# Optimization experiments

Measured on AMD Instinct MI355X. Metric: run time of the kernel, lower is better.

Reference implementation:

```python
import jax, jax.numpy as jnp
import numpy as np


def setup_inputs() -> dict:
    key = jax.random.key(0)
    ks = jax.random.split(key, 3)
    B, d_in, d_latent = 8192, 768, 12288
    x = jax.random.normal(ks[0], (B, d_in), dtype=jnp.float32)
    # kaiming_normal fan_in relu: std = sqrt(2/d_in)
    W_enc = jax.random.normal(ks[1], (d_latent, d_in), dtype=jnp.float32) * np.sqrt(2.0 / d_in)
    b_enc = jnp.zeros((d_latent,), dtype=jnp.float32)
    # xavier_normal: std = sqrt(2/(d_in+d_latent))
    W_dec = jax.random.normal(ks[2], (d_in, d_latent), dtype=jnp.float32) * np.sqrt(2.0 / (d_in + d_latent))
    b_dec = jnp.zeros((d_in,), dtype=jnp.float32)
    b_pre = jnp.zeros((d_in,), dtype=jnp.float32)
    return {"x": x, "b_pre": b_pre, "W_enc": W_enc, "b_enc": b_enc,
            "W_dec": W_dec, "b_dec": b_dec, "k": 64}


def reference(x, b_pre, W_enc, b_enc, W_dec, b_dec, k):
    # encode: a = (x - b_pre) @ W_enc.T + b_enc   -> (B, d_latent)
    x0 = x - b_pre
    a = jnp.einsum('bi,li->bl', x0, W_enc) + b_enc
    # topk activation (mode='value', nonneg=True): relu then keep k largest
    a_relu = jax.nn.relu(a)
    topk_val, topk_idx = jax.lax.top_k(a_relu, k)  # (B, k)
    B = a.shape[0]
    rows = jnp.arange(B)[:, None]
    z = jnp.zeros_like(a).at[rows, topk_idx].set(topk_val)
    # decode: x_hat = z @ W_dec.T + b_dec
    x_hat = jnp.einsum('bl,il->bi', z, W_dec) + b_dec
    return (x_hat, z, a)
```

## Files before the change

### kernel.cpp

```cpp
#include <hip/hip_runtime.h>

#define DIN 768
#define DL  12288
#define CAP 320
#define MARGIN 0.03f
#define UB 0.015f
#define UMAX 64
#define KMAX 128

typedef __attribute__((ext_vector_type(8))) _Float16 half8;
typedef __attribute__((ext_vector_type(4))) _Float16 half4v;
typedef __attribute__((ext_vector_type(4))) float f32x4;

__device__ __forceinline__ void gl_lds16(const void* g, void* s) {
  __builtin_amdgcn_global_load_lds(
      (const __attribute__((address_space(1))) unsigned int*)g,
      (__attribute__((address_space(3))) unsigned int*)s, 16, 0, 0);
}
__device__ __forceinline__ void wait_lgkm0_fence() {
  asm volatile("s_waitcnt lgkmcnt(0)" ::: "memory");
  __builtin_amdgcn_sched_barrier(0);
}
__device__ __forceinline__ void wait_vm0() {
  asm volatile("s_waitcnt vmcnt(0)" ::: "memory");
}

__global__ __launch_bounds__(256) void k_split_x(const float* __restrict__ x,
    const float* __restrict__ b_pre, _Float16* __restrict__ Ah)
{
  const int i4 = blockIdx.x * 256 + threadIdx.x;
  const int col4 = (i4 % (DIN / 4)) * 4;
  const float4 xv = *(const float4*)&x[(size_t)i4 * 4];
  const float4 bp = *(const float4*)&b_pre[col4];
  half4v o;
  o.x = (_Float16)(xv.x - bp.x);
  o.y = (_Float16)(xv.y - bp.y);
  o.z = (_Float16)(xv.z - bp.z);
  o.w = (_Float16)(xv.w - bp.w);
  *(half4v*)&Ah[(size_t)i4 * 4] = o;
}

__global__ __launch_bounds__(256) void k_split_w(const float* __restrict__ W,
                                                 _Float16* __restrict__ Bh)
{
  const int i4 = blockIdx.x * 256 + threadIdx.x;
  const float4 wv = *(const float4*)&W[(size_t)i4 * 4];
  half4v o;
  o.x = (_Float16)wv.x; o.y = (_Float16)wv.y;
  o.z = (_Float16)wv.z; o.w = (_Float16)wv.w;
  *(half4v*)&Bh[(size_t)i4 * 4] = o;
}

__global__ __launch_bounds__(256) void k_transpose(const float* __restrict__ W,
                                                   _Float16* __restrict__ WT)
{
  __shared__ float t[32][33];
  const int c0 = blockIdx.x * 32;
  const int r0 = blockIdx.y * 32;
  const int x = threadIdx.x;
  const int y = threadIdx.y;
#pragma unroll
  for (int dy = 0; dy < 32; dy += 8)
    t[y + dy][x] = W[(size_t)(r0 + y + dy) * DL + c0 + x];
  __syncthreads();
#pragma unroll
  for (int dy = 0; dy < 32; dy += 8)
    WT[(size_t)(c0 + y + dy) * DIN + r0 + x] = (_Float16)t[x][y + dy];
}

#define BM 256
#define BN 256
#define BKE 64
#define NKT (DIN / BKE)

__global__ __launch_bounds__(512) void k_encode_f16(
    const _Float16* __restrict__ Ah, const _Float16* __restrict__ Bh,
    const float* __restrict__ b_enc, float* __restrict__ aout)
{
  __shared__ _Float16 sA[2][BM][BKE];
  __shared__ _Float16 sB[2][BN][BKE];
  const int tid = threadIdx.x, wave = tid >> 6, lane = tid & 63;
  const int wm = wave >> 2, wn = wave & 3;
  const int fr = lane & 15, fc = lane >> 4;

  const int q = ((8192 / BM) * (DL / BN)) >> 3;
  const int wg = (blockIdx.x & 7) * q + (blockIdx.x >> 3);
  const int bm = (wg / (DL / BN)) * BM;
  const int bn = (wg % (DL / BN)) * BN;

  const int lrow = lane >> 3;
  const int lcol = ((lane & 7) ^ lrow) << 3;
  const _Float16* gA = Ah + (size_t)(bm + lrow) * DIN + lcol;
  const _Float16* gB = Bh + (size_t)(bn + lrow) * DIN + lcol;

  f32x4 acc[8][4];
#pragma unroll
  for (int i = 0; i < 8; ++i)
#pragma unroll
    for (int j = 0; j < 4; ++j) acc[i][j] = f32x4{0.f, 0.f, 0.f, 0.f};

#define STAGE_TILE(buf, tt)                                                      \
  {                                                                              \
    _Pragma("unroll")                                                            \
    for (int s4 = 0; s4 < 4; ++s4) {                                             \
      const int s8 = (wave + s4 * 8) * 8;                                        \
      gl_lds16(gA + (size_t)s8 * DIN + (tt) * BKE, &sA[buf][s8][0]);             \
      gl_lds16(gB + (size_t)s8 * DIN + (tt) * BKE, &sB[buf][s8][0]);             \
    }                                                                            \
  }

#define LOADQ(p, mh, nh)                                                         \
  {                                                                              \
    const char* bA = (const char*)&sA[p][0][0];                                  \
    const char* bB = (const char*)&sB[p][0][0];                                  \
    _Pragma("unroll")                                                            \
    for (int i = 0; i < 4; ++i)                                                  \
      _Pragma("unroll")                                                          \
      for (int ks = 0; ks < 2; ++ks) {                                           \
        const int row = wm * 128 + ((mh) * 4 + i) * 16 + fr;                     \
        const int ph = (ks * 4 + fc) ^ (fr & 7);                                 \
        af[i][ks] = *(const half8*)(bA + row * (BKE * 2) + ph * 16);             \
      }                                                                          \
    _Pragma("unroll")                                                            \
    for (int j = 0; j < 2; ++j)                                                  \
      _Pragma("unroll")                                                          \
      for (int ks = 0; ks < 2; ++ks) {                                           \
        const int row = wn * 64 + ((nh) * 2 + j) * 16 + fr;                      \
        const int ph = (ks * 4 + fc) ^ (fr & 7);                                 \
        bf[j][ks] = *(const half8*)(bB + row * (BKE * 2) + ph * 16);             \
      }                                                                          \
  }

#define MFMAQ(mh, nh)                                                            \
  __builtin_amdgcn_s_setprio(1);                                                 \
  _Pragma("unroll")                                                              \
  for (int i = 0; i < 4; ++i)                                                    \
    _Pragma("unroll")                                                            \
    for (int j = 0; j < 2; ++j)                                                  \
      _Pragma("unroll")                                                          \
      for (int ks = 0; ks < 2; ++ks)                                             \
        acc[(mh) * 4 + i][(nh) * 2 + j] = __builtin_amdgcn_mfma_f32_16x16x32_f16( \
            af[i][ks], bf[j][ks], acc[(mh) * 4 + i][(nh) * 2 + j], 0, 0, 0);     \
  __builtin_amdgcn_s_setprio(0);

  half8 af[4][2], bf[2][2];

  STAGE_TILE(0, 0)
  wait_vm0();
  __builtin_amdgcn_s_barrier();

#pragma unroll 1
  for (int t = 0; t < NKT; ++t) {
    const int p = t & 1;
    LOADQ(p, 0, 0)
    if (t + 1 < NKT) STAGE_TILE(p ^ 1, t + 1)
    __builtin_amdgcn_s_barrier();
    wait_lgkm0_fence();
    MFMAQ(0, 0)
    __builtin_amdgcn_s_barrier();
    LOADQ(p, 0, 1)
    __builtin_amdgcn_s_barrier();
    wait_lgkm0_fence();
    MFMAQ(0, 1)
    __builtin_amdgcn_s_barrier();
    LOADQ(p, 1, 0)
    __builtin_amdgcn_s_barrier();
    wait_lgkm0_fence();
    MFMAQ(1, 0)
    __builtin_amdgcn_s_barrier();
    LOADQ(p, 1, 1)
    wait_vm0();
    __builtin_amdgcn_s_barrier();
    wait_lgkm0_fence();
    MFMAQ(1, 1)
    __builtin_amdgcn_s_barrier();
  }

#pragma unroll
  for (int j = 0; j < 4; ++j) {
    const int col = bn + wn * 64 + j * 16 + fr;
    const float be = b_enc[col];
#pragma unroll
    for (int i = 0; i < 8; ++i) {
      const int row0 = bm + wm * 128 + i * 16 + fc * 4;
#pragma unroll
      for (int r = 0; r < 4; ++r)
        aout[(size_t)(row0 + r) * DL + col] = acc[i][j][r] + be;
    }
  }
#undef STAGE_TILE
#undef LOADQ
#undef MFMAQ
}

__global__ __launch_bounds__(256) void k_fused(
    const float* __restrict__ a, const float* __restrict__ x,
    const float* __restrict__ b_pre, const float* __restrict__ W,
    const float* __restrict__ b_enc, const int* __restrict__ kp,
    const _Float16* __restrict__ WT, const float* __restrict__ b_dec,
    float* __restrict__ z, float* __restrict__ xhat)
{
  const int row = blockIdx.x, tid = threadIdx.x;
  const int wave = tid >> 6, lane = tid & 63;
  const int kk = min(max(kp[0], 1), KMAX);
  const float* ar = a + (size_t)row * DL;
  float* zr = z + (size_t)row * DL;

  __shared__ unsigned hist[4][512];
  __shared__ float s_wmax[4];
  __shared__ unsigned s_wsuf[4];
  __shared__ float s_Tm;
  __shared__ int s_cnt;
  __shared__ int cidx[CAP];
  __shared__ float caf[CAP];
  __shared__ double x0[DIN];
  __shared__ float s_ak;
  __shared__ int s_ucnt, s_nw;
  __shared__ int uidx[UMAX];
  __shared__ double uex[UMAX];
  __shared__ int widx[KMAX];
  __shared__ float wval[KMAX];

  float4 v[12];
#pragma unroll
  for (int j = 0; j < 12; ++j) {
    float4 t4 = ((const float4*)ar)[tid + 256 * j];
    t4.x = fmaxf(t4.x, 0.f); t4.y = fmaxf(t4.y, 0.f);
    t4.z = fmaxf(t4.z, 0.f); t4.w = fmaxf(t4.w, 0.f);
    v[j] = t4;
    const float4 zz = {0.f, 0.f, 0.f, 0.f};
    ((float4*)zr)[tid + 256 * j] = zz;
  }
  float m = 0.f;
#pragma unroll
  for (int j = 0; j < 12; ++j)
    m = fmaxf(m, fmaxf(fmaxf(v[j].x, v[j].y), fmaxf(v[j].z, v[j].w)));
#pragma unroll
  for (int off = 32; off; off >>= 1) m = fmaxf(m, __shfl_xor(m, off));
  if (lane == 0) s_wmax[wave] = m;
  if (tid == 0) { s_cnt = 0; s_Tm = -1.f; s_ak = -1e30f; s_ucnt = 0; s_nw = 0; }
  __syncthreads();
  const float rmax = fmaxf(fmaxf(s_wmax[0], s_wmax[1]), fmaxf(s_wmax[2], s_wmax[3]));

  float Tm;
  if (rmax <= 0.f) {
    Tm = 1e30f;
  } else {
    const float scale = 512.f / rmax;
    unsigned need = (unsigned)kk;
    bool found = false;
    for (int phase = 0; phase < 2 && !found; ++phase) {
      for (int i = tid; i < 4 * 512; i += 256) (&hist[0][0])[i] = 0u;
      __syncthreads();
      unsigned* h = hist[wave];
      const float sc = (phase == 0) ? scale : scale * 8.f;
#pragma unroll
      for (int j = 0; j < 12; ++j) {
        const float vv[4] = {v[j].x, v[j].y, v[j].z, v[j].w};
#pragma unroll
        for (int e = 0; e < 4; ++e) {
          const float val = vv[e];
          if (val > 0.f) {
            const float fb = val * scale;
            if (phase == 0) {
              if (fb >= 64.f) atomicAdd(&h[min(511, (int)fb)], 1u);
            } else {
              if (fb < 64.f) atomicAdd(&h[min(511, (int)(val * sc))], 1u);
            }
          }
        }
      }
      __syncthreads();
      const unsigned lo = hist[0][2 * tid] + hist[1][2 * tid] + hist[2][2 * tid] + hist[3][2 * tid];
      const unsigned hi = hist[0][2 * tid + 1] + hist[1][2 * tid + 1] + hist[2][2 * tid + 1] + hist[3][2 * tid + 1];
      const unsigned st = lo + hi;
      unsigned s = st;
#pragma unroll
      for (int off = 1; off < 64; off <<= 1) {
        const unsigned o = __shfl_down(s, off);
        if (lane + off < 64) s += o;
      }
      if (lane == 0) s_wsuf[wave] = s;
      __syncthreads();
      unsigned above_w = 0;
#pragma unroll
      for (int w2 = 0; w2 < 4; ++w2) if (w2 > wave) above_w += s_wsuf[w2];
      const unsigned inc = s + above_w;
      const unsigned excl = inc - st;
      const unsigned total = s_wsuf[0] + s_wsuf[1] + s_wsuf[2] + s_wsuf[3];
      if (total >= need) {
        if (inc >= need && excl < need) {
          const int bin = (excl + hi >= need) ? (2 * tid + 1) : (2 * tid);
          s_Tm = (float)bin / sc - MARGIN;
        }
        found = true;
      } else {
        need -= total;
      }
      __syncthreads();
    }
    Tm = s_Tm;
  }

#pragma unroll
  for (int j = 0; j < 12; ++j) {
    const float vv[4] = {v[j].x, v[j].y, v[j].z, v[j].w};
#pragma unroll
    for (int e = 0; e < 4; ++e) {
      if (vv[e] > 0.f && vv[e] >= Tm) {
        const int p = atomicAdd(&s_cnt, 1);
        if (p < CAP) { cidx[p] = (tid + 256 * j) * 4 + e; caf[p] = vv[e]; }
      }
    }
  }
  for (int i = tid; i < DIN; i += 256)
    x0[i] = (double)x[(size_t)row * DIN + i] - (double)b_pre[i];
  __syncthreads();
  const int C = min(s_cnt, CAP);

  if (C > kk) {
    if (tid < C) {
      const float mv = caf[tid];
      const int mi = cidx[tid];
      int r = 0;
      for (int j = 0; j < C; ++j) {
        const float fj = caf[j];
        if (fj > mv || (fj == mv && cidx[j] < mi)) ++r;
      }
      if (r == kk - 1) s_ak = mv;
    }
    __syncthreads();
  }
  const float ak = s_ak;

  if (tid < C) {
    const float mv = caf[tid];
    if (C <= kk || mv > ak + UB) {
      const int p = atomicAdd(&s_nw, 1);
      widx[p] = cidx[tid]; wval[p] = mv;
    } else if (mv >= ak - UB) {
      const int p = atomicAdd(&s_ucnt, 1);
      if (p < UMAX) uidx[p] = cidx[tid];
    }
  }
  __syncthreads();
  const int ci = s_nw;
  const int ucnt = min(s_ucnt, UMAX);

  for (int c = wave; c < ucnt; c += 4) {
    const int idx = uidx[c];
    const float* wrow = W + (size_t)idx * DIN;
    double s = 0.0;
#pragma unroll
    for (int it = 0; it < DIN / 64; ++it)
      s = fma(x0[lane + it * 64], (double)wrow[lane + it * 64], s);
#pragma unroll
    for (int mm = 32; mm; mm >>= 1) s += __shfl_xor(s, mm);
    if (lane == 0) {
      const double e = s + (double)b_enc[idx];
      uex[c] = e > 0.0 ? e : 0.0;
    }
  }
  __syncthreads();

  const int utake = min(kk - ci, ucnt);
  if (tid < ucnt) {
    const double mv = uex[tid];
    const int mi = uidx[tid];
    int r = 0;
    for (int j = 0; j < ucnt; ++j) {
      const double fj = uex[j];
      if (fj > mv || (fj == mv && uidx[j] < mi)) ++r;
    }
    if (r < utake) {
      const int p = atomicAdd(&s_nw, 1);
      widx[p] = mi; wval[p] = (float)mv;
    }
  }
  __syncthreads();
  const int nW = s_nw;

  if (tid < nW) zr[widx[tid]] = wval[tid];

  if (tid < 192) {
    float4 acc = ((const float4*)b_dec)[tid];
    for (int j = 0; j < nW; ++j) {
      const float vv = wval[j];
      const half4v w4 = *(const half4v*)(WT + (size_t)widx[j] * DIN + tid * 4);
      acc.x = fmaf(vv, (float)w4.x, acc.x);
      acc.y = fmaf(vv, (float)w4.y, acc.y);
      acc.z = fmaf(vv, (float)w4.z, acc.z);
      acc.w = fmaf(vv, (float)w4.w, acc.w);
    }
    ((float4*)(xhat + (size_t)row * DIN))[tid] = acc;
  }
}

extern "C" void kernel_launch(void* const* d_in, const int* in_sizes, int n_in,
                              void* d_out, int out_size, void* d_ws, size_t ws_size,
                              hipStream_t stream)
{
  const float* x     = (const float*)d_in[0];
  const float* b_pre = (const float*)d_in[1];
  const float* W_enc = (const float*)d_in[2];
  const float* b_enc = (const float*)d_in[3];
  const float* W_dec = (const float*)d_in[4];
  const float* b_dec = (const float*)d_in[5];
  const int*   kp    = (const int*)d_in[6];
  const int M = in_sizes[0] / DIN;

  float* xhat = (float*)d_out;
  float* z    = xhat + (size_t)M * DIN;
  float* a    = z + (size_t)M * DL;

  const bool bigws = ws_size >= ((size_t)192 << 20);
  _Float16 *WT16, *Ah, *Bh;
  if (bigws) {
    WT16 = (_Float16*)((char*)d_ws + ((size_t)1 << 20));
    Ah   = (_Float16*)((char*)d_ws + ((size_t)64 << 20));
    Bh   = (_Float16*)((char*)d_ws + ((size_t)96 << 20));
  } else {
    WT16 = (_Float16*)z;
    Ah   = (_Float16*)(z + (size_t)12 * 1024 * 1024);
    Bh   = (_Float16*)(z + (size_t)20 * 1024 * 1024);
  }

  k_split_x<<<M * DIN / 1024, 256, 0, stream>>>(x, b_pre, Ah);
  k_split_w<<<DL * DIN / 1024, 256, 0, stream>>>(W_enc, Bh);
  k_transpose<<<dim3(DL / 32, DIN / 32), dim3(32, 8), 0, stream>>>(W_dec, WT16);
  k_encode_f16<<<(M / BM) * (DL / BN), 512, 0, stream>>>(Ah, Bh, b_enc, a);
  k_fused<<<M, 256, 0, stream>>>(a, x, b_pre, W_enc, b_enc, kp, WT16, b_dec, z, xhat);
}
```

Measured before the change: 732.1 us.

## Merge prep kernels into one launch and widen fused top-k block to 512

The three preprocessing kernels (x cast, W_enc cast, W_dec transpose) become a single launch that dispatches on block index, which removes two kernel launches and their tail gaps. The per-row fused top-k/decode kernel moves from 256 to 512 threads, so each thread holds 6 float4s instead of 12. The histogram scan now uses one bin per thread, with 8 waves sharing 4 histogram copies. This is meant to cut register pressure and per-thread serial work, at the cost of more atomic contention on the shared histograms and more block-level sync overhead.

Result: faster. 665.4 us (-9.1%).

```diff
diff --git a/kernel.cpp b/kernel.cpp
--- a/kernel.cpp
+++ b/kernel.cpp
@@ -25,47 +25,48 @@
   asm volatile("s_waitcnt vmcnt(0)" ::: "memory");
 }
 
-__global__ __launch_bounds__(256) void k_split_x(const float* __restrict__ x,
-    const float* __restrict__ b_pre, _Float16* __restrict__ Ah)
+#define NBX (8192 * DIN / 1024)
+#define NBW (DL * DIN / 1024)
+#define NBT ((DL / 32) * (DIN / 32))
+
+__global__ __launch_bounds__(256) void k_prep(
+    const float* __restrict__ x, const float* __restrict__ b_pre,
+    const float* __restrict__ W_enc, const float* __restrict__ W_dec,
+    _Float16* __restrict__ Ah, _Float16* __restrict__ Bh, _Float16* __restrict__ WT)
 {
-  const int i4 = blockIdx.x * 256 + threadIdx.x;
-  const int col4 = (i4 % (DIN / 4)) * 4;
-  const float4 xv = *(const float4*)&x[(size_t)i4 * 4];
-  const float4 bp = *(const float4*)&b_pre[col4];
-  half4v o;
-  o.x = (_Float16)(xv.x - bp.x);
-  o.y = (_Float16)(xv.y - bp.y);
-  o.z = (_Float16)(xv.z - bp.z);
-  o.w = (_Float16)(xv.w - bp.w);
-  *(half4v*)&Ah[(size_t)i4 * 4] = o;
-}
-
-__global__ __launch_bounds__(256) void k_split_w(const float* __restrict__ W,
-                                                 _Float16* __restrict__ Bh)
-{
-  const int i4 = blockIdx.x * 256 + threadIdx.x;
-  const float4 wv = *(const float4*)&W[(size_t)i4 * 4];
-  half4v o;
-  o.x = (_Float16)wv.x; o.y = (_Float16)wv.y;
-  o.z = (_Float16)wv.z; o.w = (_Float16)wv.w;
-  *(half4v*)&Bh[(size_t)i4 * 4] = o;
-}
-
-__global__ __launch_bounds__(256) void k_transpose(const float* __restrict__ W,
-                                                   _Float16* __restrict__ WT)
-{
-  __shared__ float t[32][33];
-  const int c0 = blockIdx.x * 32;
-  const int r0 = blockIdx.y * 32;
-  const int x = threadIdx.x;
-  const int y = threadIdx.y;
-#pragma unroll
-  for (int dy = 0; dy < 32; dy += 8)
-    t[y + dy][x] = W[(size_t)(r0 + y + dy) * DL + c0 + x];
-  __syncthreads();
-#pragma unroll
-  for (int dy = 0; dy < 32; dy += 8)
-    WT[(size_t)(c0 + y + dy) * DIN + r0 + x] = (_Float16)t[x][y + dy];
+  const int b = blockIdx.x, tid = threadIdx.x;
+  if (b < NBX) {
+    const int i4 = b * 256 + tid;
+    const int col4 = (i4 % (DIN / 4)) * 4;
+    const float4 xv = *(const float4*)&x[(size_t)i4 * 4];
+    const float4 bp = *(const float4*)&b_pre[col4];
+    half4v o;
+    o.x = (_Float16)(xv.x - bp.x);
+    o.y = (_Float16)(xv.y - bp.y);
+    o.z = (_Float16)(xv.z - bp.z);
+    o.w = (_Float16)(xv.w - bp.w);
+    *(half4v*)&Ah[(size_t)i4 * 4] = o;
+  } else if (b < NBX + NBW) {
+    const int i4 = (b - NBX) * 256 + tid;
+    const float4 wv = *(const float4*)&W_enc[(size_t)i4 * 4];
+    half4v o;
+    o.x = (_Float16)wv.x; o.y = (_Float16)wv.y;
+    o.z = (_Float16)wv.z; o.w = (_Float16)wv.w;
+    *(half4v*)&Bh[(size_t)i4 * 4] = o;
+  } else {
+    const int idx = b - NBX - NBW;
+    const int c0 = (idx % (DL / 32)) * 32;
+    const int r0 = (idx / (DL / 32)) * 32;
+    const int xx = tid & 31, yy = tid >> 5;
+    __shared__ float t[32][33];
+#pragma unroll
+    for (int dy = 0; dy < 32; dy += 8)
+      t[yy + dy][xx] = W_dec[(size_t)(r0 + yy + dy) * DL + c0 + xx];
+    __syncthreads();
+#pragma unroll
+    for (int dy = 0; dy < 32; dy += 8)
+      WT[(size_t)(c0 + yy + dy) * DIN + r0 + xx] = (_Float16)t[xx][yy + dy];
+  }
 }
 
 #define BM 256
@@ -193,7 +194,7 @@
 #undef MFMAQ
 }
 
-__global__ __launch_bounds__(256) void k_fused(
+__global__ __launch_bounds__(512) void k_fused(
     const float* __restrict__ a, const float* __restrict__ x,
     const float* __restrict__ b_pre, const float* __restrict__ W,
     const float* __restrict__ b_enc, const int* __restrict__ kp,
@@ -207,8 +208,8 @@
   float* zr = z + (size_t)row * DL;
 
   __shared__ unsigned hist[4][512];
-  __shared__ float s_wmax[4];
-  __shared__ unsigned s_wsuf[4];
+  __shared__ float s_wmax[8];
+  __shared__ unsigned s_wsuf[8];
   __shared__ float s_Tm;
   __shared__ int s_cnt;
   __shared__ int cidx[CAP];
@@ -221,26 +222,28 @@
   __shared__ int widx[KMAX];
   __shared__ float wval[KMAX];
 
-  float4 v[12];
-#pragma unroll
-  for (int j = 0; j < 12; ++j) {
-    float4 t4 = ((const float4*)ar)[tid + 256 * j];
+  float4 v[6];
+#pragma unroll
+  for (int j = 0; j < 6; ++j) {
+    float4 t4 = ((const float4*)ar)[tid + 512 * j];
     t4.x = fmaxf(t4.x, 0.f); t4.y = fmaxf(t4.y, 0.f);
     t4.z = fmaxf(t4.z, 0.f); t4.w = fmaxf(t4.w, 0.f);
     v[j] = t4;
     const float4 zz = {0.f, 0.f, 0.f, 0.f};
-    ((float4*)zr)[tid + 256 * j] = zz;
+    ((float4*)zr)[tid + 512 * j] = zz;
   }
   float m = 0.f;
 #pragma unroll
-  for (int j = 0; j < 12; ++j)
+  for (int j = 0; j < 6; ++j)
     m = fmaxf(m, fmaxf(fmaxf(v[j].x, v[j].y), fmaxf(v[j].z, v[j].w)));
 #pragma unroll
   for (int off = 32; off; off >>= 1) m = fmaxf(m, __shfl_xor(m, off));
   if (lane == 0) s_wmax[wave] = m;
   if (tid == 0) { s_cnt = 0; s_Tm = -1.f; s_ak = -1e30f; s_ucnt = 0; s_nw = 0; }
   __syncthreads();
-  const float rmax = fmaxf(fmaxf(s_wmax[0], s_wmax[1]), fmaxf(s_wmax[2], s_wmax[3]));
+  float rmax = s_wmax[0];
+#pragma unroll
+  for (int w2 = 1; w2 < 8; ++w2) rmax = fmaxf(rmax, s_wmax[w2]);
 
   float Tm;
   if (rmax <= 0.f) {
@@ -250,12 +253,12 @@
     unsigned need = (unsigned)kk;
     bool found = false;
     for (int phase = 0; phase < 2 && !found; ++phase) {
-      for (int i = tid; i < 4 * 512; i += 256) (&hist[0][0])[i] = 0u;
+      for (int i = tid; i < 4 * 512; i += 512) (&hist[0][0])[i] = 0u;
       __syncthreads();
-      unsigned* h = hist[wave];
+      unsigned* h = hist[wave & 3];
       const float sc = (phase == 0) ? scale : scale * 8.f;
 #pragma unroll
-      for (int j = 0; j < 12; ++j) {
+      for (int j = 0; j < 6; ++j) {
         const float vv[4] = {v[j].x, v[j].y, v[j].z, v[j].w};
 #pragma unroll
         for (int e = 0; e < 4; ++e) {
@@ -271,9 +274,7 @@
         }
       }
       __syncthreads();
-      const unsigned lo = hist[0][2 * tid] + hist[1][2 * tid] + hist[2][2 * tid] + hist[3][2 * tid];
-      const unsigned hi = hist[0][2 * tid + 1] + hist[1][2 * tid + 1] + hist[2][2 * tid + 1] + hist[3][2 * tid + 1];
-      const unsigned st = lo + hi;
+      const unsigned st = hist[0][tid] + hist[1][tid] + hist[2][tid] + hist[3][tid];
       unsigned s = st;
 #pragma unroll
       for (int off = 1; off < 64; off <<= 1) {
@@ -282,17 +283,17 @@
       }
       if (lane == 0) s_wsuf[wave] = s;
       __syncthreads();
-      unsigned above_w = 0;
-#pragma unroll
-      for (int w2 = 0; w2 < 4; ++w2) if (w2 > wave) above_w += s_wsuf[w2];
+      unsigned above_w = 0, total = 0;
+#pragma unroll
+      for (int w2 = 0; w2 < 8; ++w2) {
+        total += s_wsuf[w2];
+        if (w2 > wave) above_w += s_wsuf[w2];
+      }
       const unsigned inc = s + above_w;
       const unsigned excl = inc - st;
-      const unsigned total = s_wsuf[0] + s_wsuf[1] + s_wsuf[2] + s_wsuf[3];
       if (total >= need) {
-        if (inc >= need && excl < need) {
-          const int bin = (excl + hi >= need) ? (2 * tid + 1) : (2 * tid);
-          s_Tm = (float)bin / sc - MARGIN;
-        }
+        if (inc >= need && excl < need)
+          s_Tm = (float)tid / sc - MARGIN;
         found = true;
       } else {
         need -= total;
@@ -303,17 +304,17 @@
   }
 
 #pragma unroll
-  for (int j = 0; j < 12; ++j) {
+  for (int j = 0; j < 6; ++j) {
     const float vv[4] = {v[j].x, v[j].y, v[j].z, v[j].w};
 #pragma unroll
     for (int e = 0; e < 4; ++e) {
       if (vv[e] > 0.f && vv[e] >= Tm) {
         const int p = atomicAdd(&s_cnt, 1);
-        if (p < CAP) { cidx[p] = (tid + 256 * j) * 4 + e; caf[p] = vv[e]; }
-      }
-    }
-  }
-  for (int i = tid; i < DIN; i += 256)
+        if (p < CAP) { cidx[p] = (tid + 512 * j) * 4 + e; caf[p] = vv[e]; }
+      }
+    }
+  }
+  for (int i = tid; i < DIN; i += 512)
     x0[i] = (double)x[(size_t)row * DIN + i] - (double)b_pre[i];
   __syncthreads();
   const int C = min(s_cnt, CAP);
@@ -347,7 +348,7 @@
   const int ci = s_nw;
   const int ucnt = min(s_ucnt, UMAX);
 
-  for (int c = wave; c < ucnt; c += 4) {
+  for (int c = wave; c < ucnt; c += 8) {
     const int idx = uidx[c];
     const float* wrow = W + (size_t)idx * DIN;
     double s = 0.0;
@@ -425,9 +426,7 @@
     Bh   = (_Float16*)(z + (size_t)20 * 1024 * 1024);
   }
 
-  k_split_x<<<M * DIN / 1024, 256, 0, stream>>>(x, b_pre, Ah);
-  k_split_w<<<DL * DIN / 1024, 256, 0, stream>>>(W_enc, Bh);
-  k_transpose<<<dim3(DL / 32, DIN / 32), dim3(32, 8), 0, stream>>>(W_dec, WT16);
+  k_prep<<<NBX + NBW + NBT, 256, 0, stream>>>(x, b_pre, W_enc, W_dec, Ah, Bh, WT16);
   k_encode_f16<<<(M / BM) * (DL / BN), 512, 0, stream>>>(Ah, Bh, b_enc, a);
-  k_fused<<<M, 256, 0, stream>>>(a, x, b_pre, W_enc, b_enc, kp, WT16, b_dec, z, xhat);
-}
+  k_fused<<<M, 512, 0, stream>>>(a, x, b_pre, W_enc, b_enc, kp, WT16, b_dec, z, xhat);
+}
```
